# Optimization experiments

Hardware: AMD Instinct MI355X
Metric: run time of the kernel (lower is better)

Reference implementation:

```python
import jax, jax.numpy as jnp
import numpy as np
from jax import lax

T_ITERS = 6
LN_EPS = 1e-5

def layer_norm(x, g, b):
    mu = jnp.mean(x, axis=-1, keepdims=True)
    var = jnp.var(x, axis=-1, keepdims=True)
    return (x - mu) * lax.rsqrt(var + LN_EPS) * g + b

def setup_inputs() -> dict:
    key = jax.random.key(0)
    ks = jax.random.split(key, 12)
    B, C_in, S = 8, 128, 33
    hidden = 2 * C_in          # 256
    dim = 256                  # feat_dim
    N = 64
    w = lambda k, shp, s=0.02: (jax.random.normal(k, shp, jnp.float32) * s)
    return {
        "x": jax.random.normal(ks[0], (B, C_in, S, S, S), jnp.float32),
        "templates_init": jax.random.normal(ks[1], (1, N, dim), jnp.float32),
        "conv_w": w(ks[2], (hidden, C_in, 3, 3, 3)),
        "conv_b": jnp.zeros((hidden,), jnp.float32),
        "Wq": w(ks[3], (dim, dim)),
        "Wk": w(ks[4], (hidden, dim)),
        "Wv": w(ks[5], (hidden, dim)),
        "ln_in_g": jnp.ones((hidden,), jnp.float32), "ln_in_b": jnp.zeros((hidden,), jnp.float32),
        "ln_t_g": jnp.ones((dim,), jnp.float32),    "ln_t_b": jnp.zeros((dim,), jnp.float32),
        "ln_m_g": jnp.ones((dim,), jnp.float32),    "ln_m_b": jnp.zeros((dim,), jnp.float32),
        "W1": w(ks[6], (dim, 2 * dim)), "b1": jnp.zeros((2 * dim,), jnp.float32),
        "W2": w(ks[7], (2 * dim, dim)), "b2": jnp.zeros((dim,), jnp.float32),
    }

def reference(x, templates_init, conv_w, conv_b, Wq, Wk, Wv,
              ln_in_g, ln_in_b, ln_t_g, ln_t_b, ln_m_g, ln_m_b,
              W1, b1, W2, b2):
    # project: Conv3d stride 2, no padding, + ReLU
    h = lax.conv_general_dilated(x, conv_w, window_strides=(2, 2, 2),
                                 padding='VALID',
                                 dimension_numbers=('NCDHW', 'OIDHW', 'NCDHW'))
    h = jax.nn.relu(h + conv_b[None, :, None, None, None])
    B, C, X, Y, Z = h.shape
    dim = templates_init.shape[-1]
    N = templates_init.shape[1]
    scale = dim ** (-0.5)
    tokens = h.reshape(B, C, X * Y * Z).transpose(0, 2, 1)   # (B, L, hidden)
    tokens = layer_norm(tokens, ln_in_g, ln_in_b)
    k = tokens @ Wk                                           # (B, L, dim)
    v = tokens @ Wv                                           # (B, L, dim)
    templates = jnp.broadcast_to(templates_init, (B, N, dim))
    attn = None
    for _ in range(T_ITERS):
        t_prev = templates
        t = layer_norm(templates, ln_t_g, ln_t_b)
        q = (t @ Wq) * scale                                  # (B, N, dim)
        attn_logits = jnp.einsum('bnd,bld->bln', q, k)        # (B, L, N)
        attn = jax.nn.softmax(attn_logits, axis=-1)           # competitive over N
        attn = attn + 1e-8
        attn = attn / jnp.sum(attn, axis=-2, keepdims=True)   # renormalize over L
        templates = t_prev + jnp.einsum('bld,bln->bnd', v, attn)
        m = layer_norm(templates, ln_m_g, ln_m_b)
        templates = templates + (jax.nn.gelu(m @ W1 + b1, approximate=False) @ W2 + b2)
    templates_out = templates.transpose(0, 2, 1)              # (B, dim, N)
    attn_out = attn.transpose(0, 2, 1).reshape(B, N, X, Y, Z)
    return templates_out, attn_out
```

## Files before the change

kernel.cpp:

```cpp
#include <hip/hip_runtime.h>

typedef unsigned short u16;
typedef short s16x8 __attribute__((ext_vector_type(8)));
typedef float f32x4 __attribute__((ext_vector_type(4)));
typedef float f32x4u __attribute__((ext_vector_type(4), aligned(4)));
typedef unsigned short us4 __attribute__((ext_vector_type(4)));

__device__ __forceinline__ float bf2f(u16 v) {
    return __uint_as_float(((unsigned int)v) << 16);
}
__device__ __forceinline__ u16 f2bf(float f) {
    unsigned int u = __float_as_uint(f);
    u = u + 0x7FFFu + ((u >> 16) & 1u);
    return (u16)(u >> 16);
}
__device__ __forceinline__ f32x4 mfma16(s16x8 a, s16x8 b, f32x4 c) {
    return __builtin_amdgcn_mfma_f32_16x16x32_bf16(a, b, c, 0, 0, 0);
}
#define ZERO4 f32x4{0.f, 0.f, 0.f, 0.f}

__global__ void prepack_kernel(const float* __restrict__ conv_w, const float* __restrict__ Wk,
                               const float* __restrict__ Wv, const float* __restrict__ Wq,
                               const float* __restrict__ W1, const float* __restrict__ W2,
                               u16* __restrict__ Bp, u16* __restrict__ WkvP, u16* __restrict__ WqP,
                               u16* __restrict__ W1T, u16* __restrict__ W2T)
{
    int idx = blockIdx.x * 256 + threadIdx.x;
    if (idx < 294912) {
        int n = idx / 1152, g = idx - n * 1152;
        int ic = g / 9, r = g - ic * 9;
        const float* s = conv_w + n * 3456 + ic * 27 + r * 3;
        u16* d = Bp + n * 4608 + g * 4;
        d[0] = f2bf(s[0]); d[1] = f2bf(s[1]); d[2] = f2bf(s[2]); d[3] = 0;
    } else if (idx < 425984) {
        int i = idx - 294912;
        int n = i >> 8, c = i & 255;
        WkvP[i] = f2bf((n < 256) ? Wk[c * 256 + n] : Wv[c * 256 + (n - 256)]);
    } else if (idx < 491520) {
        int i = idx - 425984;
        int n = i >> 8, c = i & 255;
        WqP[i] = f2bf(Wq[c * 256 + n]);
    } else if (idx < 622592) {
        int i = idx - 491520;
        int h = i >> 8, c = i & 255;
        W1T[i] = f2bf(W1[c * 512 + h]);
    } else if (idx < 753664) {
        int i = idx - 622592;
        int dd = i >> 9, h = i & 511;
        W2T[i] = f2bf(W2[h * 256 + dd]);
    }
}

__global__ __launch_bounds__(512, 4) void conv_fused(
    const float* __restrict__ x, const u16* __restrict__ Bp, const float* __restrict__ conv_b,
    const float* __restrict__ ln_g, const float* __restrict__ ln_b, const u16* __restrict__ WkvP,
    u16* __restrict__ kbuf, u16* __restrict__ vT)
{
    __shared__ __align__(16) char smem[38400];
    u16* slab   = (u16*)smem;
    u16* tokbf  = (u16*)smem;
    float* lnred  = (float*)(smem + 33792);
    float* lnstat = (float*)(smem + 37888);

    int blk = blockIdx.x;
    int b = blk & 7, ox = (blk >> 5) & 15, oyb = (blk >> 3) & 3;
    int tid = threadIdx.x, wid = tid >> 6, lane = tid & 63;
    int quad = lane >> 4, l15 = lane & 15;
    int nbase = wid * 32;

    f32x4 acc[4][2];
    #pragma unroll
    for (int i = 0; i < 4; ++i)
        #pragma unroll
        for (int j = 0; j < 2; ++j) acc[i][j] = ZERO4;

    const u16* bprow0 = Bp + (nbase + l15) * 4608 + quad * 8;
    const u16* bprow1 = bprow0 + 16 * 4608;

    for (int icc = 0; icc < 8; ++icc) {
        __syncthreads();
        {
            f32x4u tv[8];
            int so8[8];
            #pragma unroll
            for (int u = 0; u < 8; ++u) {
                int s = tid + u * 512;
                tv[u] = f32x4u{0.f, 0.f, 0.f, 0.f};
                so8[u] = -1;
                if (s < 3888) {
                    int row = s / 9;
                    int c = s - row * 9;
                    int icl = row / 27;
                    int rr = row - icl * 27;
                    int ixl = rr / 9;
                    int iyl = rr - ixl * 9;
                    const float* xr = x + ((size_t)((b * 128 + icc * 16 + icl) * 33)
                                           + (2 * ox + ixl)) * 1089 + (8 * oyb + iyl) * 33;
                    if (c < 8) tv[u] = *(const f32x4u*)(xr + c * 4);
                    else       tv[u].x = xr[32];
                    so8[u] = row * 36 + c * 4;
                }
            }
            #pragma unroll
            for (int u = 0; u < 8; ++u) {
                if (so8[u] >= 0) {
                    us4 w;
                    w.x = f2bf(tv[u].x); w.y = f2bf(tv[u].y);
                    w.z = f2bf(tv[u].z); w.w = f2bf(tv[u].w);
                    *(us4*)(slab + so8[u]) = w;
                }
            }
        }
        __syncthreads();

        const u16* bk0 = bprow0 + icc * 576;
        const u16* bk1 = bprow1 + icc * 576;
        s16x8 bbA[2], bbB[2];
        bbA[0] = *reinterpret_cast<const s16x8*>(bk0);
        bbA[1] = *reinterpret_cast<const s16x8*>(bk1);

#define CONV_STEP(CC, BREG)                                                     \
        {                                                                       \
            int g = (CC) * 8 + quad * 2;                                        \
            int i0 = g / 9, r9 = g - i0 * 9;                                    \
            int kx = r9 / 3, ky = r9 - kx * 3;                                  \
            int base0 = (i0 * 27 + kx * 9 + ky) * 36 + 2 * l15;                 \
            g += 1;                                                             \
            i0 = g / 9; r9 = g - i0 * 9; kx = r9 / 3; ky = r9 - kx * 3;         \
            int base1 = (i0 * 27 + kx * 9 + ky) * 36 + 2 * l15;                 \
            _Pragma("unroll")                                                   \
            for (int fm = 0; fm < 4; ++fm) {                                    \
                union { s16x8 v; ushort2 h[4]; } af;                            \
                const u16* sp0 = slab + base0 + fm * 72;                        \
                const u16* sp1 = slab + base1 + fm * 72;                        \
                af.h[0] = *(const ushort2*)(sp0);                               \
                af.h[1] = *(const ushort2*)(sp0 + 2);                           \
                af.h[2] = *(const ushort2*)(sp1);                               \
                af.h[3] = *(const ushort2*)(sp1 + 2);                           \
                acc[fm][0] = mfma16(af.v, (BREG)[0], acc[fm][0]);               \
                acc[fm][1] = mfma16(af.v, (BREG)[1], acc[fm][1]);               \
            }                                                                   \
        }

        #pragma unroll 1
        for (int c8 = 0; c8 < 18; c8 += 2) {
            bbB[0] = *reinterpret_cast<const s16x8*>(bk0 + (c8 + 1) * 32);
            bbB[1] = *reinterpret_cast<const s16x8*>(bk1 + (c8 + 1) * 32);
            CONV_STEP(c8, bbA)
            if (c8 + 2 < 18) {
                bbA[0] = *reinterpret_cast<const s16x8*>(bk0 + (c8 + 2) * 32);
                bbA[1] = *reinterpret_cast<const s16x8*>(bk1 + (c8 + 2) * 32);
            }
            CONV_STEP(c8 + 1, bbB)
        }
#undef CONV_STEP
    }
    #pragma unroll
    for (int fn = 0; fn < 2; ++fn) {
        float bias = conv_b[nbase + fn * 16 + l15];
        #pragma unroll
        for (int fm = 0; fm < 4; ++fm)
            #pragma unroll
            for (int r = 0; r < 4; ++r)
                acc[fm][fn][r] = fmaxf(acc[fm][fn][r] + bias, 0.f);
    }
    #pragma unroll
    for (int fm = 0; fm < 4; ++fm) {
        #pragma unroll
        for (int r = 0; r < 4; ++r) {
            float s = acc[fm][0][r] + acc[fm][1][r];
            float q2 = acc[fm][0][r] * acc[fm][0][r] + acc[fm][1][r] * acc[fm][1][r];
            #pragma unroll
            for (int msk = 1; msk <= 8; msk <<= 1) {
                s  += __shfl_xor(s, msk, 64);
                q2 += __shfl_xor(q2, msk, 64);
            }
            if (l15 == 0) {
                int mm = fm * 16 + quad * 4 + r;
                lnred[(wid * 64 + mm) * 2 + 0] = s;
                lnred[(wid * 64 + mm) * 2 + 1] = q2;
            }
        }
    }
    __syncthreads();
    if (tid < 64) {
        float s = 0, q2 = 0;
        #pragma unroll
        for (int w = 0; w < 8; ++w) { s += lnred[(w * 64 + tid) * 2]; q2 += lnred[(w * 64 + tid) * 2 + 1]; }
        float mu = s * (1.f / 256.f);
        float var = fmaxf(q2 * (1.f / 256.f) - mu * mu, 0.f);
        lnstat[tid * 2]     = mu;
        lnstat[tid * 2 + 1] = rsqrtf(var + 1e-5f);
    }
    __syncthreads();
    {
        float gam[2], bet[2];
        #pragma unroll
        for (int fn = 0; fn < 2; ++fn) {
            int n = nbase + fn * 16 + l15;
            gam[fn] = ln_g[n]; bet[fn] = ln_b[n];
        }
        #pragma unroll
        for (int fm = 0; fm < 4; ++fm)
            #pragma unroll
            for (int r = 0; r < 4; ++r) {
                int mm = fm * 16 + quad * 4 + r;
                float mu = lnstat[mm * 2], rs = lnstat[mm * 2 + 1];
                #pragma unroll
                for (int fn = 0; fn < 2; ++fn) {
                    int n = nbase + fn * 16 + l15;
                    tokbf[mm * 264 + n] = f2bf((acc[fm][fn][r] - mu) * rs * gam[fn] + bet[fn]);
                }
            }
    }
    __syncthreads();
    f32x4 kacc[4][4];
    #pragma unroll
    for (int i = 0; i < 4; ++i)
        #pragma unroll
        for (int j = 0; j < 4; ++j) kacc[i][j] = ZERO4;
    int n2 = wid * 64;
    const u16* wp = WkvP + (n2 + l15) * 256 + quad * 8;
    s16x8 wvA[4], wvB[4];
    #pragma unroll
    for (int fn = 0; fn < 4; ++fn) wvA[fn] = *reinterpret_cast<const s16x8*>(wp + fn * 4096);

#define KV_STEP(KK, WREG)                                                           \
    {                                                                               \
        s16x8 a2[4];                                                                \
        _Pragma("unroll")                                                           \
        for (int fm = 0; fm < 4; ++fm)                                              \
            a2[fm] = *reinterpret_cast<const s16x8*>(tokbf + (fm * 16 + l15) * 264  \
                                                     + (KK) * 32 + quad * 8);       \
        _Pragma("unroll")                                                           \
        for (int fn = 0; fn < 4; ++fn)                                              \
            _Pragma("unroll")                                                       \
            for (int fm = 0; fm < 4; ++fm)                                          \
                kacc[fm][fn] = mfma16(a2[fm], (WREG)[fn], kacc[fm][fn]);            \
    }

    #pragma unroll 1
    for (int kc = 0; kc < 8; kc += 2) {
        #pragma unroll
        for (int fn = 0; fn < 4; ++fn)
            wvB[fn] = *reinterpret_cast<const s16x8*>(wp + fn * 4096 + (kc + 1) * 32);
        KV_STEP(kc, wvA)
        if (kc + 2 < 8) {
            #pragma unroll
            for (int fn = 0; fn < 4; ++fn)
                wvA[fn] = *reinterpret_cast<const s16x8*>(wp + fn * 4096 + (kc + 2) * 32);
        }
        KV_STEP(kc + 1, wvB)
    }
#undef KV_STEP

    #pragma unroll
    for (int fm = 0; fm < 4; ++fm)
        #pragma unroll
        for (int r = 0; r < 4; ++r) {
            int l = (ox * 16 + oyb * 4 + fm) * 16 + quad * 4 + r;
            #pragma unroll
            for (int fn = 0; fn < 4; ++fn) {
                int n = n2 + fn * 16 + l15;
                u16 v = f2bf(kacc[fm][fn][r]);
                if (n < 256) kbuf[((b << 12) + l) * 256 + n] = v;
                else         vT[((b * 256 + (n - 256)) << 12) + l] = v;
            }
        }
}

__global__ __launch_bounds__(256) void kQ(
    const float* __restrict__ tinit, float* __restrict__ tpl,
    const float* __restrict__ ln_t_g, const float* __restrict__ ln_t_b,
    const u16* __restrict__ WqP, u16* __restrict__ qbuf)
{
    __shared__ __align__(16) u16 mls[64 * 264];
    __shared__ float pls[64][4][2];
    __shared__ float stat[64][2];
    int b = blockIdx.x, tid = threadIdx.x;
    int m = tid >> 2, part = tid & 3;
    const float* tp = tinit + m * 256 + part * 64;
    float* tg = tpl + (b * 64 + m) * 256 + part * 64;
    float s = 0, q2 = 0;
    for (int i = 0; i < 64; ++i) {
        float v = tp[i];
        tg[i] = v;
        s += v; q2 += v * v;
    }
    pls[m][part][0] = s; pls[m][part][1] = q2;
    __syncthreads();
    if (tid < 64) {
        float ss = 0, qq = 0;
        #pragma unroll
        for (int p = 0; p < 4; ++p) { ss += pls[tid][p][0]; qq += pls[tid][p][1]; }
        float mu = ss * (1.f / 256.f);
        float var = fmaxf(qq * (1.f / 256.f) - mu * mu, 0.f);
        stat[tid][0] = mu; stat[tid][1] = rsqrtf(var + 1e-5f);
    }
    __syncthreads();
    {
        float mu = stat[m][0], rs = stat[m][1];
        for (int i = 0; i < 64; ++i) {
            int d = part * 64 + i;
            mls[m * 264 + d] = f2bf((tp[i] - mu) * rs * ln_t_g[d] + ln_t_b[d]);
        }
    }
    __syncthreads();
    int wid = tid >> 6, lane = tid & 63, quad = lane >> 4, l15 = lane & 15;
    f32x4 qa[4][4];
    #pragma unroll
    for (int i = 0; i < 4; ++i)
        #pragma unroll
        for (int j = 0; j < 4; ++j) qa[i][j] = ZERO4;
    #pragma unroll 1
    for (int kc = 0; kc < 8; ++kc) {
        s16x8 a[4];
        #pragma unroll
        for (int fm = 0; fm < 4; ++fm)
            a[fm] = *reinterpret_cast<const s16x8*>(mls + (fm * 16 + l15) * 264 + kc * 32 + quad * 8);
        #pragma unroll
        for (int fn = 0; fn < 4; ++fn) {
            s16x8 bv = *reinterpret_cast<const s16x8*>(WqP + (wid * 64 + fn * 16 + l15) * 256 + kc * 32 + quad * 8);
            #pragma unroll
            for (int fm = 0; fm < 4; ++fm)
                qa[fm][fn] = mfma16(a[fm], bv, qa[fm][fn]);
        }
    }
    #pragma unroll
    for (int fm = 0; fm < 4; ++fm)
        #pragma unroll
        for (int fn = 0; fn < 4; ++fn)
            #pragma unroll
            for (int r = 0; r < 4; ++r) {
                int mt = fm * 16 + quad * 4 + r;
                int d = wid * 64 + fn * 16 + l15;
                qbuf[(b * 64 + mt) * 256 + d] = f2bf(qa[fm][fn][r] * 0.0625f);
            }
}

__global__ __launch_bounds__(512, 2) void kP(
    const u16* __restrict__ qbuf, const u16* __restrict__ kbuf,
    float* __restrict__ cs_part, u16* __restrict__ attnT)
{
    __shared__ __align__(16) u16 atile[64 * 136];
    __shared__ float colsh[8][64];
    int b = blockIdx.x & 7, ltg = blockIdx.x >> 3;
    int tid = threadIdx.x, wid = tid >> 6, lane = tid & 63;
    int quad = lane >> 4, l15 = lane & 15;
    const u16* qb = qbuf + b * 16384;
    int lrow = ltg * 128 + wid * 16;
    const u16* arow = kbuf + (size_t)((b << 12) + lrow + l15) * 256;
    f32x4 sa[4];
    #pragma unroll
    for (int fn = 0; fn < 4; ++fn) sa[fn] = ZERO4;
    #pragma unroll 2
    for (int kc = 0; kc < 8; ++kc) {
        s16x8 a = *reinterpret_cast<const s16x8*>(arow + kc * 32 + quad * 8);
        #pragma unroll
        for (int fn = 0; fn < 4; ++fn) {
            s16x8 bv = *reinterpret_cast<const s16x8*>(qb + (fn * 16 + l15) * 256 + kc * 32 + quad * 8);
            sa[fn] = mfma16(a, bv, sa[fn]);
        }
    }
    float colp[4] = {0.f, 0.f, 0.f, 0.f};
    #pragma unroll
    for (int r = 0; r < 4; ++r) {
        float mx = fmaxf(fmaxf(sa[0][r], sa[1][r]), fmaxf(sa[2][r], sa[3][r]));
        #pragma unroll
        for (int msk = 1; msk <= 8; msk <<= 1) mx = fmaxf(mx, __shfl_xor(mx, msk, 64));
        float e[4], sum = 0;
        #pragma unroll
        for (int fn = 0; fn < 4; ++fn) { e[fn] = __expf(sa[fn][r] - mx); sum += e[fn]; }
        #pragma unroll
        for (int msk = 1; msk <= 8; msk <<= 1) sum += __shfl_xor(sum, msk, 64);
        float inv = 1.f / sum;
        #pragma unroll
        for (int fn = 0; fn < 4; ++fn) {
            float p = e[fn] * inv + 1e-8f;
            colp[fn] += p;
            atile[(fn * 16 + l15) * 136 + wid * 16 + quad * 4 + r] = f2bf(p);
        }
    }
    #pragma unroll
    for (int fn = 0; fn < 4; ++fn) {
        float c = colp[fn];
        c += __shfl_xor(c, 16, 64);
        c += __shfl_xor(c, 32, 64);
        if (lane < 16) colsh[wid][fn * 16 + lane] = c;
    }
    __syncthreads();
    if (tid < 64) {
        float s = 0;
        #pragma unroll
        for (int w = 0; w < 8; ++w) s += colsh[w][tid];
        cs_part[((b << 5) + ltg) * 64 + tid] = s;
    }
    {
        int n = tid >> 3, lo = (tid & 7) * 16;
        const u16* src = atile + n * 136 + lo;
        u16* dst = attnT + (size_t)((b * 64 + n) << 12) + ltg * 128 + lo;
        *(int4*)(dst)     = *(const int4*)(src);
        *(int4*)(dst + 8) = *(const int4*)(src + 8);
    }
}

__global__ __launch_bounds__(512, 2) void kPV(
    const u16* __restrict__ attnT, const u16* __restrict__ vT, float* __restrict__ delta)
{
    __shared__ float pred[8][64][16];
    int b = blockIdx.x & 7, dt = blockIdx.x >> 3;
    int tid = threadIdx.x, wid = tid >> 6, lane = tid & 63;
    int quad = lane >> 4, l15 = lane & 15;
    const u16* prow = attnT + (size_t)((b * 64 + l15) << 12) + wid * 512 + quad * 8;
    const u16* vrow = vT + (size_t)((b * 256 + dt * 16 + l15) << 12) + wid * 512 + quad * 8;
    f32x4 acc[4];
    #pragma unroll
    for (int i = 0; i < 4; ++i) acc[i] = ZERO4;
    s16x8 aA[4], bA, aB[4], bB;
    bA = *reinterpret_cast<const s16x8*>(vrow);
    #pragma unroll
    for (int fm = 0; fm < 4; ++fm) aA[fm] = *reinterpret_cast<const s16x8*>(prow + (fm << 16));
    #pragma unroll 1
    for (int kc = 0; kc < 16; kc += 2) {
        bB = *reinterpret_cast<const s16x8*>(vrow + (kc + 1) * 32);
        #pragma unroll
        for (int fm = 0; fm < 4; ++fm)
            aB[fm] = *reinterpret_cast<const s16x8*>(prow + (fm << 16) + (kc + 1) * 32);
        #pragma unroll
        for (int fm = 0; fm < 4; ++fm) acc[fm] = mfma16(aA[fm], bA, acc[fm]);
        if (kc + 2 < 16) {
            bA = *reinterpret_cast<const s16x8*>(vrow + (kc + 2) * 32);
            #pragma unroll
            for (int fm = 0; fm < 4; ++fm)
                aA[fm] = *reinterpret_cast<const s16x8*>(prow + (fm << 16) + (kc + 2) * 32);
        }
        #pragma unroll
        for (int fm = 0; fm < 4; ++fm) acc[fm] = mfma16(aB[fm], bB, acc[fm]);
    }
    #pragma unroll
    for (int fm = 0; fm < 4; ++fm)
        #pragma unroll
        for (int r = 0; r < 4; ++r)
            pred[wid][fm * 16 + quad * 4 + r][l15] = acc[fm][r];
    __syncthreads();
    for (int i = tid; i < 1024; i += 512) {
        int n = i >> 4, d = i & 15;
        float s = 0;
        #pragma unroll
        for (int w = 0; w < 8; ++w) s += pred[w][n][d];
        delta[(size_t)(b * 64 + n) * 256 + dt * 16 + d] = s;
    }
}

__global__ __launch_bounds__(256) void kT(
    float* __restrict__ tpl, const float* __restrict__ delta, const float* __restrict__ cs_part,
    float* __restrict__ colsum,
    const float* __restrict__ ln_m_g, const float* __restrict__ ln_m_b,
    const u16* __restrict__ W1T, const float* __restrict__ b1,
    const u16* __restrict__ W2T, const float* __restrict__ b2,
    const float* __restrict__ ln_t_g, const float* __restrict__ ln_t_b,
    const u16* __restrict__ WqP, u16* __restrict__ qbuf,
    int last, float* __restrict__ out0)
{
    __shared__ __align__(16) u16 mls[16 * 264];
    __shared__ __align__(16) u16 hid[16 * 520];
    __shared__ float pls[16][16][2];
    __shared__ float stat[16][2];
    __shared__ float lnr2[4][16][2];
    __shared__ float csh[16];
    int b = blockIdx.x & 7, mg = blockIdx.x >> 3;
    int m0 = mg * 16;
    int tid = threadIdx.x, wid = tid >> 6, lane = tid & 63;
    int quad = lane >> 4, l15 = lane & 15;
    if (tid < 16) {
        float s = 0;
        #pragma unroll
        for (int g = 0; g < 32; ++g) s += cs_part[((b << 5) + g) * 64 + m0 + tid];
        csh[tid] = 1.f / s;
        if (last) colsum[b * 64 + m0 + tid] = s;
    }
    __syncthreads();
    {
        int ml = tid >> 4, part = tid & 15;
        float cinv = csh[ml];
        float* tg = tpl + (b * 64 + m0 + ml) * 256 + part * 16;
        const float* dg = delta + (b * 64 + m0 + ml) * 256 + part * 16;
        float vbuf[16];
        float s = 0, q2 = 0;
        #pragma unroll
        for (int i = 0; i < 16; ++i) {
            float v = tg[i] + dg[i] * cinv;
            vbuf[i] = v; s += v; q2 += v * v;
        }
        pls[ml][part][0] = s; pls[ml][part][1] = q2;
        __syncthreads();
        if (tid < 16) {
            float ss = 0, qq = 0;
            #pragma unroll
            for (int p = 0; p < 16; ++p) { ss += pls[tid][p][0]; qq += pls[tid][p][1]; }
            float mu = ss * (1.f / 256.f);
            float var = fmaxf(qq * (1.f / 256.f) - mu * mu, 0.f);
            stat[tid][0] = mu; stat[tid][1] = rsqrtf(var + 1e-5f);
        }
        __syncthreads();
        float mu = stat[ml][0], rs = stat[ml][1];
        #pragma unroll
        for (int i = 0; i < 16; ++i) {
            int d = part * 16 + i;
            tg[i] = vbuf[i];
            mls[ml * 264 + d] = f2bf((vbuf[i] - mu) * rs * ln_m_g[d] + ln_m_b[d]);
        }
    }
    __syncthreads();
    {
        f32x4 ha[8];
        #pragma unroll
        for (int j = 0; j < 8; ++j) ha[j] = ZERO4;
        #pragma unroll 1
        for (int kc = 0; kc < 8; ++kc) {
            s16x8 a = *reinterpret_cast<const s16x8*>(mls + l15 * 264 + kc * 32 + quad * 8);
            #pragma unroll
            for (int fn = 0; fn < 8; ++fn) {
                s16x8 bv = *reinterpret_cast<const s16x8*>(W1T + (wid * 128 + fn * 16 + l15) * 256 + kc * 32 + quad * 8);
                ha[fn] = mfma16(a, bv, ha[fn]);
            }
        }
        #pragma unroll
        for (int fn = 0; fn < 8; ++fn) {
            int nh = wid * 128 + fn * 16 + l15;
            float bb = b1[nh];
            #pragma unroll
            for (int r = 0; r < 4; ++r) {
                float v = ha[fn][r] + bb;
                v = 0.5f * v * (1.f + erff(v * 0.70710678118654752f));
                hid[(quad * 4 + r) * 520 + nh] = f2bf(v);
            }
        }
    }
    __syncthreads();
    {
        f32x4 oa[4];
        #pragma unroll
        for (int j = 0; j < 4; ++j) oa[j] = ZERO4;
        #pragma unroll 1
        for (int kc = 0; kc < 16; ++kc) {
            s16x8 a = *reinterpret_cast<const s16x8*>(hid + l15 * 520 + kc * 32 + quad * 8);
            #pragma unroll
            for (int fn = 0; fn < 4; ++fn) {
                s16x8 bv = *reinterpret_cast<const s16x8*>(W2T + (wid * 64 + fn * 16 + l15) * 512 + kc * 32 + quad * 8);
                oa[fn] = mfma16(a, bv, oa[fn]);
            }
        }
        #pragma unroll
        for (int fn = 0; fn < 4; ++fn) {
            int d = wid * 64 + fn * 16 + l15;
            float bb = b2[d];
            #pragma unroll
            for (int r = 0; r < 4; ++r) {
                int mm = quad * 4 + r;
                oa[fn][r] += bb + tpl[(b * 64 + m0 + mm) * 256 + d];
            }
        }
        #pragma unroll
        for (int r = 0; r < 4; ++r) {
            float s = oa[0][r] + oa[1][r] + oa[2][r] + oa[3][r];
            float q2 = oa[0][r] * oa[0][r] + oa[1][r] * oa[1][r]
                     + oa[2][r] * oa[2][r] + oa[3][r] * oa[3][r];
            #pragma unroll
            for (int msk = 1; msk <= 8; msk <<= 1) {
                s  += __shfl_xor(s, msk, 64);
                q2 += __shfl_xor(q2, msk, 64);
            }
            if (l15 == 0) {
                lnr2[wid][quad * 4 + r][0] = s;
                lnr2[wid][quad * 4 + r][1] = q2;
            }
        }
        __syncthreads();
        if (tid < 16) {
            float ss = 0, qq = 0;
            #pragma unroll
            for (int w = 0; w < 4; ++w) { ss += lnr2[w][tid][0]; qq += lnr2[w][tid][1]; }
            float mu = ss * (1.f / 256.f);
            float var = fmaxf(qq * (1.f / 256.f) - mu * mu, 0.f);
            stat[tid][0] = mu; stat[tid][1] = rsqrtf(var + 1e-5f);
        }
        __syncthreads();
        #pragma unroll
        for (int fn = 0; fn < 4; ++fn) {
            int d = wid * 64 + fn * 16 + l15;
            float gg = last ? 0.f : ln_t_g[d];
            float bt = last ? 0.f : ln_t_b[d];
            #pragma unroll
            for (int r = 0; r < 4; ++r) {
                int mm = quad * 4 + r;
                float v = oa[fn][r];
                tpl[(b * 64 + m0 + mm) * 256 + d] = v;
                if (last) {
                    out0[(b * 256 + d) * 64 + m0 + mm] = v;
                } else {
                    mls[mm * 264 + d] = f2bf((v - stat[mm][0]) * stat[mm][1] * gg + bt);
                }
            }
        }
    }
    if (!last) {
        __syncthreads();
        f32x4 qa[4];
        #pragma unroll
        for (int j = 0; j < 4; ++j) qa[j] = ZERO4;
        #pragma unroll 1
        for (int kc = 0; kc < 8; ++kc) {
            s16x8 a = *reinterpret_cast<const s16x8*>(mls + l15 * 264 + kc * 32 + quad * 8);
            #pragma unroll
            for (int fn = 0; fn < 4; ++fn) {
                s16x8 bv = *reinterpret_cast<const s16x8*>(WqP + (wid * 64 + fn * 16 + l15) * 256 + kc * 32 + quad * 8);
                qa[fn] = mfma16(a, bv, qa[fn]);
            }
        }
        #pragma unroll
        for (int fn = 0; fn < 4; ++fn)
            #pragma unroll
            for (int r = 0; r < 4; ++r) {
                int mt = m0 + quad * 4 + r;
                int d = wid * 64 + fn * 16 + l15;
                qbuf[(b * 64 + mt) * 256 + d] = f2bf(qa[fn][r] * 0.0625f);
            }
    }
}

__global__ void kE(const u16* __restrict__ attnT, const float* __restrict__ colsum,
                   float* __restrict__ out1)
{
    int blk = blockIdx.x;
    int b = blk & 7, r8 = blk >> 3;
    int e = (b << 18) + (r8 << 10) + threadIdx.x * 4;
    int n = (e >> 12) & 63;
    float ci = 1.f / colsum[b * 64 + n];
    const u16* s = attnT + e;
    f32x4 o;
    o.x = bf2f(s[0]) * ci; o.y = bf2f(s[1]) * ci;
    o.z = bf2f(s[2]) * ci; o.w = bf2f(s[3]) * ci;
    *(f32x4*)(out1 + e) = o;
}

extern "C" void kernel_launch(void* const* d_in, const int* in_sizes, int n_in,
                              void* d_out, int out_size, void* d_ws, size_t ws_size,
                              hipStream_t stream)
{
    const float* x       = (const float*)d_in[0];
    const float* tinit   = (const float*)d_in[1];
    const float* conv_w  = (const float*)d_in[2];
    const float* conv_b  = (const float*)d_in[3];
    const float* Wq      = (const float*)d_in[4];
    const float* Wk      = (const float*)d_in[5];
    const float* Wv      = (const float*)d_in[6];
    const float* ln_in_g = (const float*)d_in[7];
    const float* ln_in_b = (const float*)d_in[8];
    const float* ln_t_g  = (const float*)d_in[9];
    const float* ln_t_b  = (const float*)d_in[10];
    const float* ln_m_g  = (const float*)d_in[11];
    const float* ln_m_b  = (const float*)d_in[12];
    const float* W1      = (const float*)d_in[13];
    const float* b1      = (const float*)d_in[14];
    const float* W2      = (const float*)d_in[15];
    const float* b2      = (const float*)d_in[16];

    char* ws = (char*)d_ws;
    u16* Bp       = (u16*)(ws + 0);
    u16* WkvP     = (u16*)(ws + 2359296);
    u16* WqP      = (u16*)(ws + 2621440);
    u16* W1T      = (u16*)(ws + 2752512);
    u16* W2T      = (u16*)(ws + 3014656);
    u16* kbuf     = (u16*)(ws + 3276800);
    u16* vT       = (u16*)(ws + 20054016);
    u16* qbuf     = (u16*)(ws + 36831232);
    u16* attnT    = (u16*)(ws + 37093376);
    float* colsum = (float*)(ws + 41287680);
    float* tpl    = (float*)(ws + 41289728);
    float* delta  = (float*)(ws + 41814016);
    float* cs_part= (float*)(ws + 42338304);

    float* out0 = (float*)d_out;
    float* out1 = out0 + 131072;

    prepack_kernel<<<2944, 256, 0, stream>>>(conv_w, Wk, Wv, Wq, W1, W2, Bp, WkvP, WqP, W1T, W2T);
    conv_fused<<<512, 512, 0, stream>>>(x, Bp, conv_b, ln_in_g, ln_in_b, WkvP, kbuf, vT);
    kQ<<<8, 256, 0, stream>>>(tinit, tpl, ln_t_g, ln_t_b, WqP, qbuf);
    for (int it = 0; it < 6; ++it) {
        int last = (it == 5) ? 1 : 0;
        kP<<<256, 512, 0, stream>>>(qbuf, kbuf, cs_part, attnT);
        kPV<<<128, 512, 0, stream>>>(attnT, vT, delta);
        kT<<<32, 256, 0, stream>>>(tpl, delta, cs_part, colsum, ln_m_g, ln_m_b, W1T, b1, W2T, b2,
                                   ln_t_g, ln_t_b, WqP, qbuf, last, out0);
    }
    kE<<<2048, 256, 0, stream>>>(attnT, colsum, out1);
}
```

Before: 806.3 us.

## Fuse attention softmax and PV product into one kernel with atomic accumulation

Merges the logits/softmax kernel and the attention-times-V kernel into a single kernel. Each block computes its 128-row attention tile, keeps it in shared memory, multiplies it by the matching slice of V and atomically adds the partial result into delta. Delta is zeroed up front and again after each consume. The attention matrix is now written to global memory only on the last iteration, and Q is staged in shared memory. This removes one launch per iteration and the global round trip of the attention tensor, at the cost of many float atomics and a non-deterministic summation order.

```diff
diff --git a/kernel.cpp b/kernel.cpp
--- a/kernel.cpp
+++ b/kernel.cpp
@@ -272,7 +272,7 @@
 __global__ __launch_bounds__(256) void kQ(
     const float* __restrict__ tinit, float* __restrict__ tpl,
     const float* __restrict__ ln_t_g, const float* __restrict__ ln_t_b,
-    const u16* __restrict__ WqP, u16* __restrict__ qbuf)
+    const u16* __restrict__ WqP, u16* __restrict__ qbuf, float* __restrict__ delta)
 {
     __shared__ __align__(16) u16 mls[64 * 264];
     __shared__ float pls[64][4][2];
@@ -336,30 +336,45 @@
                 int d = wid * 64 + fn * 16 + l15;
                 qbuf[(b * 64 + mt) * 256 + d] = f2bf(qa[fm][fn][r] * 0.0625f);
             }
-}
-
-__global__ __launch_bounds__(512, 2) void kP(
-    const u16* __restrict__ qbuf, const u16* __restrict__ kbuf,
-    float* __restrict__ cs_part, u16* __restrict__ attnT)
+    f32x4* dz = (f32x4*)(delta + b * 16384);
+    for (int i = tid; i < 4096; i += 256) dz[i] = ZERO4;
+}
+
+__global__ __launch_bounds__(512, 2) void kA(
+    const u16* __restrict__ qbuf, const u16* __restrict__ kbuf, const u16* __restrict__ vT,
+    float* __restrict__ cs_part, float* __restrict__ delta, int last, u16* __restrict__ attnT)
 {
+    __shared__ __align__(16) u16 qls[64 * 264];
     __shared__ __align__(16) u16 atile[64 * 136];
     __shared__ float colsh[8][64];
     int b = blockIdx.x & 7, ltg = blockIdx.x >> 3;
     int tid = threadIdx.x, wid = tid >> 6, lane = tid & 63;
     int quad = lane >> 4, l15 = lane & 15;
-    const u16* qb = qbuf + b * 16384;
+
+    {
+        int r = tid >> 3, c = (tid & 7) * 32;
+        const u16* src = qbuf + b * 16384 + r * 256 + c;
+        u16* dst = qls + r * 264 + c;
+        #pragma unroll
+        for (int j = 0; j < 4; ++j)
+            *(int4*)(dst + j * 8) = *(const int4*)(src + j * 8);
+    }
     int lrow = ltg * 128 + wid * 16;
     const u16* arow = kbuf + (size_t)((b << 12) + lrow + l15) * 256;
+    s16x8 av[8];
+    #pragma unroll
+    for (int kc = 0; kc < 8; ++kc)
+        av[kc] = *reinterpret_cast<const s16x8*>(arow + kc * 32 + quad * 8);
+    __syncthreads();
     f32x4 sa[4];
     #pragma unroll
     for (int fn = 0; fn < 4; ++fn) sa[fn] = ZERO4;
-    #pragma unroll 2
+    #pragma unroll
     for (int kc = 0; kc < 8; ++kc) {
-        s16x8 a = *reinterpret_cast<const s16x8*>(arow + kc * 32 + quad * 8);
         #pragma unroll
         for (int fn = 0; fn < 4; ++fn) {
-            s16x8 bv = *reinterpret_cast<const s16x8*>(qb + (fn * 16 + l15) * 256 + kc * 32 + quad * 8);
-            sa[fn] = mfma16(a, bv, sa[fn]);
+            s16x8 bv = *reinterpret_cast<const s16x8*>(qls + (fn * 16 + l15) * 264 + kc * 32 + quad * 8);
+            sa[fn] = mfma16(av[kc], bv, sa[fn]);
         }
     }
     float colp[4] = {0.f, 0.f, 0.f, 0.f};
@@ -396,6 +411,40 @@
         cs_part[((b << 5) + ltg) * 64 + tid] = s;
     }
     {
+        const u16* vrow = vT + ((size_t)(b * 256 + wid * 32 + l15) << 12) + ltg * 128 + quad * 8;
+        s16x8 bv2[2][4];
+        #pragma unroll
+        for (int fn = 0; fn < 2; ++fn)
+            #pragma unroll
+            for (int kc = 0; kc < 4; ++kc)
+                bv2[fn][kc] = *reinterpret_cast<const s16x8*>(vrow + (fn << 16) + kc * 32);
+        f32x4 pacc[4][2];
+        #pragma unroll
+        for (int i = 0; i < 4; ++i)
+            #pragma unroll
+            for (int j = 0; j < 2; ++j) pacc[i][j] = ZERO4;
+        #pragma unroll
+        for (int kc = 0; kc < 4; ++kc) {
+            #pragma unroll
+            for (int fm = 0; fm < 4; ++fm) {
+                s16x8 a = *reinterpret_cast<const s16x8*>(atile + (fm * 16 + l15) * 136 + kc * 32 + quad * 8);
+                #pragma unroll
+                for (int fn = 0; fn < 2; ++fn)
+                    pacc[fm][fn] = mfma16(a, bv2[fn][kc], pacc[fm][fn]);
+            }
+        }
+        #pragma unroll
+        for (int fm = 0; fm < 4; ++fm)
+            #pragma unroll
+            for (int fn = 0; fn < 2; ++fn)
+                #pragma unroll
+                for (int r = 0; r < 4; ++r) {
+                    int n = fm * 16 + quad * 4 + r;
+                    int d = wid * 32 + fn * 16 + l15;
+                    atomicAdd(&delta[(size_t)(b * 64 + n) * 256 + d], pacc[fm][fn][r]);
+                }
+    }
+    if (last) {
         int n = tid >> 3, lo = (tid & 7) * 16;
         const u16* src = atile + n * 136 + lo;
         u16* dst = attnT + (size_t)((b * 64 + n) << 12) + ltg * 128 + lo;
@@ -404,56 +453,8 @@
     }
 }
 
-__global__ __launch_bounds__(512, 2) void kPV(
-    const u16* __restrict__ attnT, const u16* __restrict__ vT, float* __restrict__ delta)
-{
-    __shared__ float pred[8][64][16];
-    int b = blockIdx.x & 7, dt = blockIdx.x >> 3;
-    int tid = threadIdx.x, wid = tid >> 6, lane = tid & 63;
-    int quad = lane >> 4, l15 = lane & 15;
-    const u16* prow = attnT + (size_t)((b * 64 + l15) << 12) + wid * 512 + quad * 8;
-    const u16* vrow = vT + (size_t)((b * 256 + dt * 16 + l15) << 12) + wid * 512 + quad * 8;
-    f32x4 acc[4];
-    #pragma unroll
-    for (int i = 0; i < 4; ++i) acc[i] = ZERO4;
-    s16x8 aA[4], bA, aB[4], bB;
-    bA = *reinterpret_cast<const s16x8*>(vrow);
-    #pragma unroll
-    for (int fm = 0; fm < 4; ++fm) aA[fm] = *reinterpret_cast<const s16x8*>(prow + (fm << 16));
-    #pragma unroll 1
-    for (int kc = 0; kc < 16; kc += 2) {
-        bB = *reinterpret_cast<const s16x8*>(vrow + (kc + 1) * 32);
-        #pragma unroll
-        for (int fm = 0; fm < 4; ++fm)
-            aB[fm] = *reinterpret_cast<const s16x8*>(prow + (fm << 16) + (kc + 1) * 32);
-        #pragma unroll
-        for (int fm = 0; fm < 4; ++fm) acc[fm] = mfma16(aA[fm], bA, acc[fm]);
-        if (kc + 2 < 16) {
-            bA = *reinterpret_cast<const s16x8*>(vrow + (kc + 2) * 32);
-            #pragma unroll
-            for (int fm = 0; fm < 4; ++fm)
-                aA[fm] = *reinterpret_cast<const s16x8*>(prow + (fm << 16) + (kc + 2) * 32);
-        }
-        #pragma unroll
-        for (int fm = 0; fm < 4; ++fm) acc[fm] = mfma16(aB[fm], bB, acc[fm]);
-    }
-    #pragma unroll
-    for (int fm = 0; fm < 4; ++fm)
-        #pragma unroll
-        for (int r = 0; r < 4; ++r)
-            pred[wid][fm * 16 + quad * 4 + r][l15] = acc[fm][r];
-    __syncthreads();
-    for (int i = tid; i < 1024; i += 512) {
-        int n = i >> 4, d = i & 15;
-        float s = 0;
-        #pragma unroll
-        for (int w = 0; w < 8; ++w) s += pred[w][n][d];
-        delta[(size_t)(b * 64 + n) * 256 + dt * 16 + d] = s;
-    }
-}
-
 __global__ __launch_bounds__(256) void kT(
-    float* __restrict__ tpl, const float* __restrict__ delta, const float* __restrict__ cs_part,
+    float* __restrict__ tpl, float* __restrict__ delta, const float* __restrict__ cs_part,
     float* __restrict__ colsum,
     const float* __restrict__ ln_m_g, const float* __restrict__ ln_m_b,
     const u16* __restrict__ W1T, const float* __restrict__ b1,
@@ -484,13 +485,18 @@
         int ml = tid >> 4, part = tid & 15;
         float cinv = csh[ml];
         float* tg = tpl + (b * 64 + m0 + ml) * 256 + part * 16;
-        const float* dg = delta + (b * 64 + m0 + ml) * 256 + part * 16;
+        float* dg = delta + (size_t)(b * 64 + m0 + ml) * 256 + part * 16;
         float vbuf[16];
         float s = 0, q2 = 0;
         #pragma unroll
         for (int i = 0; i < 16; ++i) {
             float v = tg[i] + dg[i] * cinv;
             vbuf[i] = v; s += v; q2 += v * v;
+        }
+        if (!last) {
+            f32x4* dz = (f32x4*)dg;
+            #pragma unroll
+            for (int i = 0; i < 4; ++i) dz[i] = ZERO4;
         }
         pls[ml][part][0] = s; pls[ml][part][1] = q2;
         __syncthreads();
@@ -686,11 +692,10 @@
 
     prepack_kernel<<<2944, 256, 0, stream>>>(conv_w, Wk, Wv, Wq, W1, W2, Bp, WkvP, WqP, W1T, W2T);
     conv_fused<<<512, 512, 0, stream>>>(x, Bp, conv_b, ln_in_g, ln_in_b, WkvP, kbuf, vT);
-    kQ<<<8, 256, 0, stream>>>(tinit, tpl, ln_t_g, ln_t_b, WqP, qbuf);
+    kQ<<<8, 256, 0, stream>>>(tinit, tpl, ln_t_g, ln_t_b, WqP, qbuf, delta);
     for (int it = 0; it < 6; ++it) {
         int last = (it == 5) ? 1 : 0;
-        kP<<<256, 512, 0, stream>>>(qbuf, kbuf, cs_part, attnT);
-        kPV<<<128, 512, 0, stream>>>(attnT, vT, delta);
+        kA<<<256, 512, 0, stream>>>(qbuf, kbuf, vT, cs_part, delta, last, attnT);
         kT<<<32, 256, 0, stream>>>(tpl, delta, cs_part, colsum, ln_m_g, ln_m_b, W1T, b1, W2T, b2,
                                    ln_t_g, ln_t_b, WqP, qbuf, last, out0);
     }
```

Measured after the change: 749.1 us. -7.1%, faster.
